# Performance work log

Measured on AMD Instinct MI355X. Metric: run time of the kernel, lower is better.

The kernel has to match this reference:

```python
import jax, jax.numpy as jnp
import numpy as np

L_OUT, B, N, C, M, D, T = 4, 4, 1000, 80, 64, 256, 28
CLS_W, L1_W, GIOU_W, MASK_W = 2.0, 5.0, 2.0, 5.0
ALPHA, GAMMA, EPS = 0.25, 2.0, 1e-8
CANDIDATE_K, CENTER_RADIUS, BIG = 10, 2.5, 100000.0


def _areas(b):
    return (b[..., 2] - b[..., 0]) * (b[..., 3] - b[..., 1])


def pairwise_giou(b1, b2):
    # b1 [n,4], b2 [m,4] -> [n,m] generalized IoU (torchvision convention)
    area1, area2 = _areas(b1), _areas(b2)
    lt = jnp.maximum(b1[:, None, :2], b2[None, :, :2])
    rb = jnp.minimum(b1[:, None, 2:], b2[None, :, 2:])
    wh = jnp.clip(rb - lt, 0.0)
    inter = wh[..., 0] * wh[..., 1]
    union = area1[:, None] + area2[None, :] - inter
    iou = inter / union
    lti = jnp.minimum(b1[:, None, :2], b2[None, :, :2])
    rbi = jnp.maximum(b1[:, None, 2:], b2[None, :, 2:])
    whi = jnp.clip(rbi - lti, 0.0)
    areai = whi[..., 0] * whi[..., 1]
    return iou - (areai - union) / areai


def diag_giou(b1, b2):
    # elementwise giou for matched pairs, b1/b2 [n,4] -> [n]
    area1, area2 = _areas(b1), _areas(b2)
    lt = jnp.maximum(b1[:, :2], b2[:, :2])
    rb = jnp.minimum(b1[:, 2:], b2[:, 2:])
    wh = jnp.clip(rb - lt, 0.0)
    inter = wh[:, 0] * wh[:, 1]
    union = area1 + area2 - inter
    iou = inter / union
    lti = jnp.minimum(b1[:, :2], b2[:, :2])
    rbi = jnp.maximum(b1[:, 2:], b2[:, 2:])
    whi = jnp.clip(rbi - lti, 0.0)
    areai = whi[:, 0] * whi[:, 1]
    return iou - (areai - union) / areai


def pairwise_iou(b1, b2, eps=1e-8):
    # mmdet bbox_overlaps, mode='iou'
    area1, area2 = _areas(b1), _areas(b2)
    lt = jnp.maximum(b1[:, None, :2], b2[None, :, :2])
    rb = jnp.minimum(b1[:, None, 2:], b2[None, :, 2:])
    wh = jnp.clip(rb - lt, 0.0)
    inter = wh[..., 0] * wh[..., 1]
    union = jnp.maximum(area1[:, None] + area2[None, :] - inter, eps)
    return inter / union


def simota_match(logits, boxes, gt_cls, gt_boxes, img_size):
    # SimOTA assignment for one image; fixed shapes via masking instead of boolean indexing
    n, c = logits.shape
    m = gt_boxes.shape[0]
    cx = (boxes[:, 0] + boxes[:, 2]) * 0.5
    cy = (boxes[:, 1] + boxes[:, 3]) * 0.5
    w = boxes[:, 2] - boxes[:, 0]
    h = boxes[:, 3] - boxes[:, 1]
    in_gt = ((cx[:, None] > gt_boxes[None, :, 0]) & (cy[:, None] > gt_boxes[None, :, 1])
             & (cx[:, None] < gt_boxes[None, :, 2]) & (cy[:, None] < gt_boxes[None, :, 3]))
    gcx = (gt_boxes[:, 0] + gt_boxes[:, 2]) * 0.5
    gcy = (gt_boxes[:, 1] + gt_boxes[:, 3]) * 0.5
    rx = CENTER_RADIUS * w[:, None]
    ry = CENTER_RADIUS * h[:, None]
    in_ct = ((cx[:, None] > gcx[None, :] - rx) & (cx[:, None] < gcx[None, :] + rx)
             & (cy[:, None] > gcy[None, :] - ry) & (cy[:, None] < gcy[None, :] + ry))
    valid = in_gt.any(1) | in_ct.any(1)
    in_both = in_gt & in_ct
    has_valid = valid.any()
    valid = valid | (~has_valid)          # fallback: all valid when none
    in_both = in_both | (~has_valid)
    # FocalLossCost (mmdet), weight = cls weight
    p = jax.nn.sigmoid(logits)
    neg = -jnp.log(1.0 - p + EPS) * (1.0 - ALPHA) * p ** GAMMA
    pos = -jnp.log(p + EPS) * ALPHA * (1.0 - p) ** GAMMA
    cls_cost = CLS_W * (pos - neg)[:, gt_cls]          # [n,m]
    nb = boxes / img_size
    ngb = gt_boxes / img_size
    l1_cost = L1_W * jnp.abs(nb[:, None, :] - ngb[None, :, :]).sum(-1)
    giou_cost = GIOU_W * (1.0 - pairwise_giou(nb, ngb))
    cost = cls_cost + l1_cost + giou_cost + (~in_both) * BIG
    cost = jnp.where(valid[:, None], cost, 1e15)       # invalid priors never selected
    ious = pairwise_iou(boxes, gt_boxes) * valid[:, None]
    # dynamic_k_matching
    topk_ious, _ = jax.lax.top_k(ious.T, CANDIDATE_K)  # [m,10]
    dyn_k = jnp.maximum(topk_ious.sum(-1).astype(jnp.int32), 1)
    rank = jnp.argsort(jnp.argsort(cost, axis=0), axis=0)
    matching = rank < dyn_k[None, :]                   # [n,m]
    multi = matching.sum(1) > 1
    best = jnp.argmin(cost, axis=1)
    best_oh = best[:, None] == jnp.arange(m)[None, :]
    matching = jnp.where(multi[:, None], best_oh, matching)
    fg = matching.any(1)
    gt_ind = jnp.argmax(matching, axis=1)
    return fg, gt_ind


def per_image_loss(logits, boxes, pfeat, gt_cls, gt_boxes, gt_masks, img_size, w_mask):
    sg = jax.lax.stop_gradient
    fg, gt_ind = simota_match(sg(logits), sg(boxes), gt_cls, sg(gt_boxes), sg(img_size))
    c = logits.shape[1]
    gcls = gt_cls[gt_ind]
    label = jnp.where(fg[:, None], jax.nn.one_hot(gcls, c, dtype=logits.dtype), 0.0)
    # sigmoid focal loss (sum over all n*c logits)
    p = jax.nn.sigmoid(logits)
    ce = -(label * jax.nn.log_sigmoid(logits) + (1.0 - label) * jax.nn.log_sigmoid(-logits))
    p_t = p * label + (1.0 - p) * (1.0 - label)
    alpha_t = ALPHA * label + (1.0 - ALPHA) * (1.0 - label)
    cls_loss = (alpha_t * ce * (1.0 - p_t) ** GAMMA).sum()
    fgf = fg.astype(logits.dtype)
    nb = boxes / img_size
    gb = gt_boxes[gt_ind] / img_size
    l1_loss = (jnp.abs(nb - gb).sum(-1) * fgf).sum()
    giou_loss = ((1.0 - diag_giou(nb, gb)) * fgf).sum()
    # mask head: per-class mask logits from proposal feats; gather only assigned class
    d = pfeat.shape[1]
    tt = T * T
    w_sel = w_mask.reshape(d, c, tt)[:, gcls, :]        # [d,n,tt]
    m_sel = jax.nn.sigmoid(jnp.einsum('nd,dnt->nt', pfeat, w_sel))
    gm = gt_masks.reshape(gt_masks.shape[0], -1)[gt_ind]  # [n,tt]
    inter = (m_sel * gm).sum(-1)
    union = m_sel.sum(-1) + gm.sum(-1) + 1e-8
    mask_loss = ((1.0 - 2.0 * inter / union) * fgf).sum()
    return cls_loss, l1_loss, giou_loss, mask_loss, fgf.sum()


def _forward(pred_logits, pred_boxes, proposal_feat, gt_boxes, gt_masks, image_size, w_mask, gt_classes):
    per = jax.vmap(per_image_loss, in_axes=(0, 0, 0, 0, 0, 0, 0, None))
    total = jnp.zeros(4, dtype=pred_logits.dtype)
    n_out = pred_logits.shape[0]
    for l in range(n_out):   # small fixed loop over output heads
        cl, l1, gl, ml, k = per(pred_logits[l], pred_boxes[l], proposal_feat[l],
                                gt_classes, gt_boxes, gt_masks, image_size, w_mask)
        num_ins = k.sum()
        total = total + jnp.stack([cl.sum(), l1.sum(), gl.sum(), ml.sum()]) / num_ins
    weights = jnp.array([CLS_W, L1_W, GIOU_W, MASK_W], dtype=total.dtype)
    return weights * total / n_out   # [cls, l1, giou, mask] losses


def setup_inputs():
    key = jax.random.key(0)
    ks = jax.random.split(key, 8)

    def rand_boxes(k, shape):
        k1, k2 = jax.random.split(k)
        ctr = jax.random.uniform(k1, shape + (2,), minval=100.0, maxval=700.0)
        wh = jax.random.uniform(k2, shape + (2,), minval=20.0, maxval=300.0)
        return jnp.concatenate([ctr - wh * 0.5, ctr + wh * 0.5], axis=-1)

    pred_logits = jax.random.normal(ks[0], (L_OUT, B, N, C), dtype=jnp.float32)
    pred_boxes = rand_boxes(ks[1], (L_OUT, B, N))
    proposal_feat = 0.1 * jax.random.normal(ks[2], (L_OUT, B, N, D), dtype=jnp.float32)
    gt_boxes = rand_boxes(ks[3], (B, M))
    gt_masks = (jax.random.uniform(ks[4], (B, M, T, T)) > 0.5).astype(jnp.float32)
    image_size = 800.0 * jnp.ones((B,), dtype=jnp.float32)
    w_mask = 0.02 * jax.random.normal(ks[5], (D, C * T * T), dtype=jnp.float32)
    gt_classes = jax.random.randint(ks[6], (B, M), 0, C)
    return {"pred_logits": pred_logits, "pred_boxes": pred_boxes, "proposal_feat": proposal_feat,
            "gt_boxes": gt_boxes, "gt_masks": gt_masks, "image_size": image_size,
            "w_mask": w_mask, "gt_classes": gt_classes}


def reference(pred_logits, pred_boxes, proposal_feat, gt_boxes, gt_masks, image_size, w_mask, gt_classes):
    return _forward(pred_logits, pred_boxes, proposal_feat, gt_boxes, gt_masks, image_size, w_mask, gt_classes)
```

## Files before the change

### kernel.cpp

```cpp
#include <hip/hip_runtime.h>
#include <math.h>
#include <float.h>

#define LOUT 4
#define BATCH 4
#define NP 1000
#define NC 80
#define NM 64
#define ND 256
#define TT 784
#define NIMG (LOUT*BATCH)
#define CWTT (NC*TT)
#define MAXF (NIMG*NP)
#define CH 32
#define TPT 112
#define MAXCH 408

__device__ __forceinline__ float block_reduce_sum(float v, float* red) {
    int tid = threadIdx.x;
    red[tid] = v; __syncthreads();
    for (int s = blockDim.x >> 1; s > 0; s >>= 1) {
        if (tid < s) red[tid] += red[tid + s];
        __syncthreads();
    }
    float r = red[0]; __syncthreads();
    return r;
}

__global__ void k_valid(const float* __restrict__ boxes, const float* __restrict__ gtb,
                        int* __restrict__ valid, unsigned long long* __restrict__ inboth,
                        int* __restrict__ hasvalid) {
    int img = blockIdx.y;
    int b = img % BATCH;
    int i = blockIdx.x * blockDim.x + threadIdx.x;
    __shared__ float g[NM * 4];
    for (int k = threadIdx.x; k < NM * 4; k += blockDim.x) g[k] = gtb[b * NM * 4 + k];
    __syncthreads();
    if (i >= NP) return;
    float4 bx = *(const float4*)&boxes[((size_t)img * NP + i) * 4];
    float x0 = bx.x, y0 = bx.y, x1 = bx.z, y1 = bx.w;
    float cx = (x0 + x1) * 0.5f, cy = (y0 + y1) * 0.5f;
    float w = x1 - x0, h = y1 - y0;
    float rx = 2.5f * w, ry = 2.5f * h;
    bool any_gt = false, any_ct = false;
    unsigned long long ib = 0ull;
    for (int j = 0; j < NM; ++j) {
        float gx0 = g[j*4], gy0 = g[j*4+1], gx1 = g[j*4+2], gy1 = g[j*4+3];
        bool igt = (cx > gx0) && (cy > gy0) && (cx < gx1) && (cy < gy1);
        float gcx = (gx0 + gx1) * 0.5f, gcy = (gy0 + gy1) * 0.5f;
        bool ict = (cx > gcx - rx) && (cx < gcx + rx) && (cy > gcy - ry) && (cy < gcy + ry);
        any_gt |= igt; any_ct |= ict;
        if (igt && ict) ib |= (1ull << j);
    }
    bool v = any_gt || any_ct;
    valid[img * NP + i] = v ? 1 : 0;
    inboth[img * NP + i] = ib;
    if (v) atomicOr(&hasvalid[img], 1);
}

__global__ void __launch_bounds__(256) k_costtopk(
        const float* __restrict__ logits, const float* __restrict__ boxes,
        const float* __restrict__ gtb, const int* __restrict__ gcls_all,
        const float* __restrict__ imsz,
        const int* __restrict__ valid, const unsigned long long* __restrict__ inboth,
        const int* __restrict__ hasvalid,
        float* __restrict__ cost, float* __restrict__ kthc, int* __restrict__ kthi) {
    int j = blockIdx.x, img = blockIdx.y, b = img % BATCH;
    float s = imsz[b], inv_s = 1.f / s;
    const float* gj = gtb + (b * NM + j) * 4;
    float gx0 = gj[0], gy0 = gj[1], gx1 = gj[2], gy1 = gj[3];
    int gc = gcls_all[b * NM + j];
    int hv = hasvalid[img];
    float garea = (gx1 - gx0) * (gy1 - gy0);
    float ngx0 = gx0 * inv_s, ngy0 = gy0 * inv_s, ngx1 = gx1 * inv_s, ngy1 = gy1 * inv_s;
    float ngarea = (ngx1 - ngx0) * (ngy1 - ngy0);
    size_t colbase = ((size_t)img * NM + j) * NP;
    int tid = threadIdx.x;
    float icv[4], ccv[4];
    #pragma unroll
    for (int e = 0; e < 4; ++e) {
        int i = tid + 256 * e;
        if (i < NP) {
            float4 bx = *(const float4*)&boxes[((size_t)img * NP + i) * 4];
            float x0 = bx.x, y0 = bx.y, x1 = bx.z, y1 = bx.w;
            float area = (x1 - x0) * (y1 - y0);
            float ltx = fmaxf(x0, gx0), lty = fmaxf(y0, gy0);
            float rbx = fminf(x1, gx1), rby = fminf(y1, gy1);
            float iw = fmaxf(rbx - ltx, 0.f), ih = fmaxf(rby - lty, 0.f);
            float inter = iw * ih;
            float uni = fmaxf(area + garea - inter, 1e-8f);
            float iou = inter / uni;
            float nx0 = x0 * inv_s, ny0 = y0 * inv_s, nx1 = x1 * inv_s, ny1 = y1 * inv_s;
            float narea = (nx1 - nx0) * (ny1 - ny0);
            float nltx = fmaxf(nx0, ngx0), nlty = fmaxf(ny0, ngy0);
            float nrbx = fminf(nx1, ngx1), nrby = fminf(ny1, ngy1);
            float niw = fmaxf(nrbx - nltx, 0.f), nih = fmaxf(nrby - nlty, 0.f);
            float ninter = niw * nih;
            float nuni = narea + ngarea - ninter;
            float niou = ninter / nuni;
            float ex0 = fminf(nx0, ngx0), ey0 = fminf(ny0, ngy0);
            float ex1 = fmaxf(nx1, ngx1), ey1 = fmaxf(ny1, ngy1);
            float earea = fmaxf(ex1 - ex0, 0.f) * fmaxf(ey1 - ey0, 0.f);
            float giou = niou - (earea - nuni) / earea;
            float giou_cost = 2.f * (1.f - giou);
            float l1 = 5.f * (fabsf(nx0 - ngx0) + fabsf(ny0 - ngy0) + fabsf(nx1 - ngx1) + fabsf(ny1 - ngy1));
            float x = logits[((size_t)img * NP + i) * NC + gc];
            float p = 1.f / (1.f + expf(-x));
            float neg = -logf(1.f - p + 1e-8f) * 0.75f * p * p;
            float pos = -logf(p + 1e-8f) * 0.25f * (1.f - p) * (1.f - p);
            float cls = 2.f * (pos - neg);
            bool vld = (valid[img * NP + i] != 0) || (hv == 0);
            bool inb = (((inboth[img * NP + i] >> j) & 1ull) != 0ull) || (hv == 0);
            float cst = cls + l1 + giou_cost + (inb ? 0.f : 100000.f);
            if (!vld) cst = 1e15f;
            cost[colbase + i] = cst;
            ccv[e] = cst;
            icv[e] = vld ? iou : 0.f;
        } else {
            ccv[e] = FLT_MAX;
            icv[e] = -FLT_MAX;
        }
    }
    __shared__ float wv[4]; __shared__ int wi[4];
    int wave = tid >> 6, lane = tid & 63;
    unsigned cons = 0;
    float ssum = 0.f;
    for (int it = 0; it < 10; ++it) {
        float bv = -FLT_MAX; int bi = NP;
        #pragma unroll
        for (int e = 0; e < 4; ++e) {
            int i = tid + 256 * e;
            float v = icv[e];
            if (!(cons & (1u << e)) && ((v > bv) || (v == bv && i < bi))) { bv = v; bi = i; }
        }
        #pragma unroll
        for (int sft = 1; sft < 64; sft <<= 1) {
            float ov = __shfl_xor(bv, sft, 64);
            int oi = __shfl_xor(bi, sft, 64);
            if ((ov > bv) || (ov == bv && oi < bi)) { bv = ov; bi = oi; }
        }
        if (lane == 0) { wv[wave] = bv; wi[wave] = bi; }
        __syncthreads();
        float gv = wv[0]; int gi = wi[0];
        #pragma unroll
        for (int w = 1; w < 4; ++w) {
            float ov = wv[w]; int oi = wi[w];
            if ((ov > gv) || (ov == gv && oi < gi)) { gv = ov; gi = oi; }
        }
        __syncthreads();
        ssum += gv;
        if ((gi & 255) == tid) cons |= (1u << (gi >> 8));
    }
    int dk = (int)ssum; if (dk < 1) dk = 1;
    cons = 0;
    float gvf = 0.f; int gif = 0;
    for (int it = 0; it < dk; ++it) {
        float bv = FLT_MAX; int bi = NP;
        #pragma unroll
        for (int e = 0; e < 4; ++e) {
            int i = tid + 256 * e;
            float v = ccv[e];
            if (!(cons & (1u << e)) && ((v < bv) || (v == bv && i < bi))) { bv = v; bi = i; }
        }
        #pragma unroll
        for (int sft = 1; sft < 64; sft <<= 1) {
            float ov = __shfl_xor(bv, sft, 64);
            int oi = __shfl_xor(bi, sft, 64);
            if ((ov < bv) || (ov == bv && oi < bi)) { bv = ov; bi = oi; }
        }
        if (lane == 0) { wv[wave] = bv; wi[wave] = bi; }
        __syncthreads();
        float gv = wv[0]; int gi = wi[0];
        #pragma unroll
        for (int w = 1; w < 4; ++w) {
            float ov = wv[w]; int oi = wi[w];
            if ((ov < gv) || (ov == gv && oi < gi)) { gv = ov; gi = oi; }
        }
        __syncthreads();
        if ((gi & 255) == tid) cons |= (1u << (gi >> 8));
        gvf = gv; gif = gi;
    }
    if (tid == 0) { kthc[blockIdx.y * NM + j] = gvf; kthi[blockIdx.y * NM + j] = gif; }
}

__global__ void k_match(const float* __restrict__ cost,
                        const float* __restrict__ kthc, const int* __restrict__ kthi,
                        const float* __restrict__ boxes, const float* __restrict__ gtb,
                        const float* __restrict__ imsz, const int* __restrict__ gcls_all,
                        int* __restrict__ fg, int* __restrict__ gt_ind,
                        int* __restrict__ cnt, float* __restrict__ accum) {
    int img = blockIdx.y, b = img % BATCH;
    int i = blockIdx.x * blockDim.x + threadIdx.x;
    __shared__ float skc[NM]; __shared__ int ski[NM];
    __shared__ float red[256];
    if (threadIdx.x < NM) {
        skc[threadIdx.x] = kthc[img * NM + threadIdx.x];
        ski[threadIdx.x] = kthi[img * NM + threadIdx.x];
    }
    __syncthreads();
    float l1 = 0.f, gl = 0.f, f = 0.f;
    if (i < NP) {
        int cntm = 0, first = -1;
        float bc = FLT_MAX; int bj = 0;
        for (int j = 0; j < NM; ++j) {
            float c = cost[((size_t)img * NM + j) * NP + i];
            bool m = (c < skc[j]) || (c == skc[j] && i <= ski[j]);
            if (m) { cntm++; if (first < 0) first = j; }
            if (c < bc) { bc = c; bj = j; }
        }
        int gi = 0, isfg = 0;
        if (cntm > 1) { gi = bj; isfg = 1; }
        else if (cntm == 1) { gi = first; isfg = 1; }
        fg[img * NP + i] = isfg;
        gt_ind[img * NP + i] = gi;
        if (isfg) {
            atomicAdd(&cnt[gcls_all[b * NM + gi]], 1);
            float inv = 1.f / imsz[b];
            float4 bx = *(const float4*)&boxes[((size_t)img * NP + i) * 4];
            const float* gj = gtb + (b * NM + gi) * 4;
            float nx0 = bx.x*inv, ny0 = bx.y*inv, nx1 = bx.z*inv, ny1 = bx.w*inv;
            float gx0 = gj[0]*inv, gy0 = gj[1]*inv, gx1 = gj[2]*inv, gy1 = gj[3]*inv;
            l1 = fabsf(nx0-gx0) + fabsf(ny0-gy0) + fabsf(nx1-gx1) + fabsf(ny1-gy1);
            float a1 = (nx1-nx0)*(ny1-ny0), a2 = (gx1-gx0)*(gy1-gy0);
            float ltx = fmaxf(nx0,gx0), lty = fmaxf(ny0,gy0);
            float rbx = fminf(nx1,gx1), rby = fminf(ny1,gy1);
            float iw = fmaxf(rbx-ltx,0.f), ih = fmaxf(rby-lty,0.f);
            float inter = iw*ih, uni = a1+a2-inter, iou = inter/uni;
            float ex0 = fminf(nx0,gx0), ey0 = fminf(ny0,gy0);
            float ex1 = fmaxf(nx1,gx1), ey1 = fmaxf(ny1,gy1);
            float ea = fmaxf(ex1-ex0,0.f)*fmaxf(ey1-ey0,0.f);
            float giou = iou - (ea-uni)/ea;
            gl = 1.f - giou;
            f = 1.f;
        }
    }
    float sl1 = block_reduce_sum(l1, red);
    float sgl = block_reduce_sum(gl, red);
    float sf  = block_reduce_sum(f, red);
    if (threadIdx.x == 0) {
        atomicAdd(&accum[img*5+1], sl1);
        atomicAdd(&accum[img*5+2], sgl);
        atomicAdd(&accum[img*5+4], sf);
    }
}

__global__ void k_focal(const float* __restrict__ logits, const int* __restrict__ fg,
                        const int* __restrict__ gt_ind, const int* __restrict__ gcls_all,
                        float* __restrict__ accum) {
    int img = blockIdx.y, b = img % BATCH;
    int idx = blockIdx.x * blockDim.x + threadIdx.x;
    __shared__ float red[256];
    float v = 0.f;
    if (idx < NP * NC) {
        int i = idx / NC, c = idx % NC;
        float x = logits[(size_t)img * NP * NC + idx];
        int lab = 0;
        if (fg[img * NP + i]) {
            int gc = gcls_all[b * NM + gt_ind[img * NP + i]];
            lab = (c == gc) ? 1 : 0;
        }
        float p = 1.f / (1.f + expf(-x));
        float ax = fabsf(x);
        float sp = log1pf(expf(-ax));
        float ls_pos = fminf(x, 0.f) - sp;
        float ls_neg = fminf(-x, 0.f) - sp;
        if (lab) v = 0.25f * (-ls_pos) * (1.f - p) * (1.f - p);
        else     v = 0.75f * (-ls_neg) * p * p;
    }
    float sv = block_reduce_sum(v, red);
    if (threadIdx.x == 0) atomicAdd(&accum[img*5+0], sv);
}

__global__ void k_gmsum(const float* __restrict__ gtm, float* __restrict__ gmsum) {
    int bj = blockIdx.x;
    __shared__ float red[128];
    float s = 0.f;
    for (int t = threadIdx.x; t < TT; t += 128) s += gtm[(size_t)bj * TT + t];
    int tid = threadIdx.x;
    red[tid] = s; __syncthreads();
    for (int st = 64; st > 0; st >>= 1) {
        if (tid < st) red[tid] += red[tid + st];
        __syncthreads();
    }
    if (tid == 0) gmsum[bj] = red[0];
}

__global__ void __launch_bounds__(1024) k_scanscatter(
        const int* __restrict__ cnt, const int* __restrict__ fg,
        const int* __restrict__ gti, const int* __restrict__ gcls,
        int* __restrict__ offs_g, int* __restrict__ total,
        int* __restrict__ chtab, int* __restrict__ nch, int* __restrict__ list) {
    __shared__ int offs[NC]; __shared__ int choff[NC]; __shared__ int sfill[NC];
    int tid = threadIdx.x;
    if (tid == 0) {
        int s = 0, m = 0;
        for (int c = 0; c < NC; ++c) {
            offs[c] = s; s += cnt[c];
            choff[c] = m; m += (cnt[c] + CH - 1) / CH;
        }
        *total = s; *nch = m;
    }
    if (tid < NC) sfill[tid] = 0;
    __syncthreads();
    if (tid < NC) {
        offs_g[tid] = offs[tid];
        int n = cnt[tid], co = choff[tid];
        for (int k = 0; k * CH < n; ++k) chtab[co + k] = (tid << 16) | k;
    }
    for (int idx = tid; idx < NIMG * NP; idx += 1024) {
        if (fg[idx]) {
            int img = idx / NP, i = idx % NP, b = img % BATCH;
            int gt = gti[idx];
            int c = gcls[b * NM + gt];
            int pos = offs[c] + atomicAdd(&sfill[c], 1);
            list[pos] = (img << 16) | (gt << 10) | i;
        }
    }
}

__global__ void __launch_bounds__(128) k_mgemm(
        const float* __restrict__ pfeat, const float* __restrict__ wmask,
        const float* __restrict__ gtm, const int* __restrict__ list,
        const int* __restrict__ cnt, const int* __restrict__ offs,
        const int* __restrict__ chtab, const int* __restrict__ nch,
        float* __restrict__ inter, float* __restrict__ msum) {
    int ch = blockIdx.x;
    if (ch >= *nch) return;
    int e = chtab[ch];
    int c = e >> 16, k = e & 0xffff;
    int base = offs[c] + k * CH;
    int P = min(CH, cnt[c] - k * CH);
    int tid = threadIdx.x;
    bool act = (tid < TPT);
    int t = blockIdx.y * TPT + (act ? tid : 0);
    __shared__ float pf[CH][ND];
    __shared__ int sl[CH];
    if (tid < CH) sl[tid] = (tid < P) ? list[base + tid] : 0;
    __syncthreads();
    for (int idx = tid; idx < CH * (ND / 4); idx += 128) {
        int p = idx >> 6, d4 = idx & 63;
        float4 v = {0.f, 0.f, 0.f, 0.f};
        if (p < P) {
            int pk = sl[p];
            int img = pk >> 16, i = pk & 1023;
            v = *(const float4*)&pfeat[((size_t)img * NP + i) * ND + d4 * 4];
        }
        *(float4*)&pf[p][d4 * 4] = v;
    }
    __syncthreads();
    float acc[CH];
    #pragma unroll
    for (int p = 0; p < CH; ++p) acc[p] = 0.f;
    if (act) {
        const float* wr = wmask + (size_t)c * TT + t;
        float4 wq[4];
        #pragma unroll
        for (int q = 0; q < 4; ++q) {
            const float* wp = wr + (size_t)q * 4 * CWTT;
            wq[q].x = wp[0]; wq[q].y = wp[CWTT];
            wq[q].z = wp[2 * (size_t)CWTT]; wq[q].w = wp[3 * (size_t)CWTT];
        }
        #pragma unroll 4
        for (int d4 = 0; d4 < 60; ++d4) {
            float4 w = wq[d4 & 3];
            const float* wp = wr + (size_t)(d4 + 4) * 4 * CWTT;
            wq[d4 & 3].x = wp[0]; wq[d4 & 3].y = wp[CWTT];
            wq[d4 & 3].z = wp[2 * (size_t)CWTT]; wq[d4 & 3].w = wp[3 * (size_t)CWTT];
            int d = d4 * 4;
            #pragma unroll
            for (int p = 0; p < CH; ++p) {
                float4 q4 = *(const float4*)&pf[p][d];
                acc[p] += q4.x * w.x + q4.y * w.y + q4.z * w.z + q4.w * w.w;
            }
        }
        #pragma unroll
        for (int d4 = 60; d4 < 64; ++d4) {
            float4 w = wq[d4 & 3];
            int d = d4 * 4;
            #pragma unroll
            for (int p = 0; p < CH; ++p) {
                float4 q4 = *(const float4*)&pf[p][d];
                acc[p] += q4.x * w.x + q4.y * w.y + q4.z * w.z + q4.w * w.w;
            }
        }
    }
    #pragma unroll 4
    for (int p = 0; p < CH; ++p) {
        if (p >= P) break;
        int pk = sl[p];
        int img = pk >> 16, j = (pk >> 10) & 63, b = img % BATCH;
        float li = 0.f, lm = 0.f;
        if (act) {
            float m = 1.f / (1.f + expf(-acc[p]));
            float g = gtm[((size_t)(b * NM + j)) * TT + t];
            li = m * g; lm = m;
        }
        #pragma unroll
        for (int s = 32; s > 0; s >>= 1) {
            li += __shfl_down(li, s, 64);
            lm += __shfl_down(lm, s, 64);
        }
        if ((tid & 63) == 0) {
            atomicAdd(&inter[base + p], li);
            atomicAdd(&msum[base + p], lm);
        }
    }
}

__global__ void __launch_bounds__(256) k_dicefinal(
        const int* __restrict__ list, const int* __restrict__ total,
        const float* __restrict__ inter, const float* __restrict__ msum,
        const float* __restrict__ gmsum, const float* __restrict__ accum,
        float* __restrict__ out) {
    __shared__ float md[NIMG];
    int tid = threadIdx.x;
    if (tid < NIMG) md[tid] = 0.f;
    __syncthreads();
    int n = *total;
    for (int e = tid; e < n; e += 256) {
        int pk = list[e];
        int img = pk >> 16, j = (pk >> 10) & 63, b = img % BATCH;
        float d = 1.f - 2.f * inter[e] / (msum[e] + gmsum[b * NM + j] + 1e-8f);
        atomicAdd(&md[img], d);
    }
    __syncthreads();
    if (tid == 0) {
        float tot[4] = {0.f, 0.f, 0.f, 0.f};
        for (int l = 0; l < LOUT; ++l) {
            float s0 = 0.f, s1 = 0.f, s2 = 0.f, s3 = 0.f, s4 = 0.f;
            for (int b = 0; b < BATCH; ++b) {
                int img = l * BATCH + b;
                s0 += accum[img*5+0]; s1 += accum[img*5+1]; s2 += accum[img*5+2];
                s3 += md[img];        s4 += accum[img*5+4];
            }
            tot[0] += s0 / s4; tot[1] += s1 / s4; tot[2] += s2 / s4; tot[3] += s3 / s4;
        }
        const float w[4] = {2.f, 5.f, 2.f, 5.f};
        for (int k = 0; k < 4; ++k) out[k] = w[k] * tot[k] / (float)LOUT;
    }
}

extern "C" void kernel_launch(void* const* d_in, const int* in_sizes, int n_in,
                              void* d_out, int out_size, void* d_ws, size_t ws_size,
                              hipStream_t stream) {
    const float* logits = (const float*)d_in[0];
    const float* boxes  = (const float*)d_in[1];
    const float* pfeat  = (const float*)d_in[2];
    const float* gtb    = (const float*)d_in[3];
    const float* gtm    = (const float*)d_in[4];
    const float* imsz   = (const float*)d_in[5];
    const float* wmask  = (const float*)d_in[6];
    const int*   gcls   = (const int*)d_in[7];

    char* ws = (char*)d_ws;
    size_t off = 0;
    auto alloc = [&](size_t bytes) -> void* {
        void* p = ws + off;
        off = (off + bytes + 255) & ~(size_t)255;
        return p;
    };
    char* zbase = ws;
    float* accum = (float*)alloc(NIMG * 5 * sizeof(float));
    int* cnt    = (int*)alloc(NC * sizeof(int));
    int* hasvalid = (int*)alloc(NIMG * sizeof(int));
    float* interA = (float*)alloc((size_t)MAXF * sizeof(float));
    float* msumA  = (float*)alloc((size_t)MAXF * sizeof(float));
    size_t zbytes = off;
    float* cost = (float*)alloc((size_t)NIMG * NM * NP * sizeof(float));
    int* valid  = (int*)alloc((size_t)NIMG * NP * sizeof(int));
    unsigned long long* inboth = (unsigned long long*)alloc((size_t)NIMG * NP * sizeof(unsigned long long));
    float* kthc = (float*)alloc(NIMG * NM * sizeof(float));
    int* kthi   = (int*)alloc(NIMG * NM * sizeof(int));
    int* fg     = (int*)alloc((size_t)NIMG * NP * sizeof(int));
    int* gti    = (int*)alloc((size_t)NIMG * NP * sizeof(int));
    float* gmsum = (float*)alloc(BATCH * NM * sizeof(float));
    int* offs   = (int*)alloc(NC * sizeof(int));
    int* total  = (int*)alloc(sizeof(int));
    int* nch    = (int*)alloc(sizeof(int));
    int* chtab  = (int*)alloc((size_t)MAXCH * sizeof(int));
    int* list   = (int*)alloc((size_t)MAXF * sizeof(int));

    hipMemsetAsync(zbase, 0, zbytes, stream);

    k_gmsum<<<BATCH * NM, 128, 0, stream>>>(gtm, gmsum);
    k_valid<<<dim3((NP + 255) / 256, NIMG), 256, 0, stream>>>(boxes, gtb, valid, inboth, hasvalid);
    k_costtopk<<<dim3(NM, NIMG), 256, 0, stream>>>(logits, boxes, gtb, gcls, imsz, valid, inboth, hasvalid, cost, kthc, kthi);
    k_match<<<dim3((NP + 255) / 256, NIMG), 256, 0, stream>>>(cost, kthc, kthi, boxes, gtb, imsz, gcls, fg, gti, cnt, accum);
    k_focal<<<dim3((NP * NC + 255) / 256, NIMG), 256, 0, stream>>>(logits, fg, gti, gcls, accum);
    k_scanscatter<<<1, 1024, 0, stream>>>(cnt, fg, gti, gcls, offs, total, chtab, nch, list);
    k_mgemm<<<dim3(MAXCH, (TT + TPT - 1) / TPT), 128, 0, stream>>>(pfeat, wmask, gtm, list, cnt, offs, chtab, nch, interA, msumA);
    k_dicefinal<<<1, 256, 0, stream>>>(list, total, interA, msumA, gmsum, accum, (float*)d_out);
}
```

Measured before the change: 237.4 us.

## Split mask GEMM over feature dim, add parallel dice reduce and transposed logits

```diff
diff --git a/kernel.cpp b/kernel.cpp
--- a/kernel.cpp
+++ b/kernel.cpp
@@ -12,9 +12,10 @@
 #define NIMG (LOUT*BATCH)
 #define CWTT (NC*TT)
 #define MAXF (NIMG*NP)
-#define CH 32
+#define CAPF 10240
+#define CH 16
 #define TPT 112
-#define MAXCH 408
+#define MAXCH 768
 
 __device__ __forceinline__ float block_reduce_sum(float v, float* red) {
     int tid = threadIdx.x;
@@ -58,8 +59,22 @@
     if (v) atomicOr(&hasvalid[img], 1);
 }
 
+__global__ void k_logT(const float* __restrict__ logits, float* __restrict__ logT) {
+    __shared__ float tile[32][33];
+    int img = blockIdx.z;
+    int i0 = blockIdx.x * 32, c0 = blockIdx.y * 32;
+    int tx = threadIdx.x, ty = threadIdx.y;
+    int i = i0 + ty, c = c0 + tx;
+    float v = 0.f;
+    if (i < NP && c < NC) v = logits[((size_t)img * NP + i) * NC + c];
+    tile[ty][tx] = v;
+    __syncthreads();
+    int co = c0 + ty, io = i0 + tx;
+    if (co < NC && io < NP) logT[((size_t)img * NC + co) * NP + io] = tile[tx][ty];
+}
+
 __global__ void __launch_bounds__(256) k_costtopk(
-        const float* __restrict__ logits, const float* __restrict__ boxes,
+        const float* __restrict__ logT, const float* __restrict__ boxes,
         const float* __restrict__ gtb, const int* __restrict__ gcls_all,
         const float* __restrict__ imsz,
         const int* __restrict__ valid, const unsigned long long* __restrict__ inboth,
@@ -75,6 +90,7 @@
     float ngx0 = gx0 * inv_s, ngy0 = gy0 * inv_s, ngx1 = gx1 * inv_s, ngy1 = gy1 * inv_s;
     float ngarea = (ngx1 - ngx0) * (ngy1 - ngy0);
     size_t colbase = ((size_t)img * NM + j) * NP;
+    const float* lrow = logT + ((size_t)img * NC + gc) * NP;
     int tid = threadIdx.x;
     float icv[4], ccv[4];
     #pragma unroll
@@ -104,7 +120,7 @@
             float giou = niou - (earea - nuni) / earea;
             float giou_cost = 2.f * (1.f - giou);
             float l1 = 5.f * (fabsf(nx0 - ngx0) + fabsf(ny0 - ngy0) + fabsf(nx1 - ngx1) + fabsf(ny1 - ngy1));
-            float x = logits[((size_t)img * NP + i) * NC + gc];
+            float x = lrow[i];
             float p = 1.f / (1.f + expf(-x));
             float neg = -logf(1.f - p + 1e-8f) * 0.75f * p * p;
             float pos = -logf(p + 1e-8f) * 0.25f * (1.f - p) * (1.f - p);
@@ -318,7 +334,125 @@
     }
 }
 
-__global__ void __launch_bounds__(128) k_mgemm(
+template<int DQ>
+__global__ void __launch_bounds__(128) k_mgemmQ(
+        const float* __restrict__ pfeat, const float* __restrict__ wmask,
+        const int* __restrict__ list, const int* __restrict__ cnt,
+        const int* __restrict__ offs, const int* __restrict__ chtab,
+        const int* __restrict__ nch, float* __restrict__ part) {
+    constexpr int DL = ND / DQ;
+    constexpr int NSTEP = DL / 4;
+    int ch = blockIdx.x;
+    if (ch >= *nch) return;
+    int e = chtab[ch];
+    int c = e >> 16, k = e & 0xffff;
+    int base = offs[c] + k * CH;
+    int P = min(CH, cnt[c] - k * CH);
+    int tid = threadIdx.x;
+    int q = blockIdx.z;
+    int dbase = q * DL;
+    bool act = (tid < TPT);
+    int t = blockIdx.y * TPT + (act ? tid : 0);
+    __shared__ float pf[CH][DL];
+    __shared__ int sl[CH];
+    if (tid < CH) sl[tid] = (tid < P) ? list[base + tid] : 0;
+    __syncthreads();
+    for (int idx = tid; idx < CH * (DL / 4); idx += 128) {
+        int p = idx / (DL / 4), d4 = idx % (DL / 4);
+        float4 v = {0.f, 0.f, 0.f, 0.f};
+        if (p < P) {
+            int pk = sl[p];
+            int img = pk >> 16, i = pk & 1023;
+            v = *(const float4*)&pfeat[((size_t)img * NP + i) * ND + dbase + d4 * 4];
+        }
+        *(float4*)&pf[p][d4 * 4] = v;
+    }
+    __syncthreads();
+    float acc[CH];
+    #pragma unroll
+    for (int p = 0; p < CH; ++p) acc[p] = 0.f;
+    if (act) {
+        const float* wr = wmask + (size_t)dbase * CWTT + (size_t)c * TT + t;
+        float4 wq[4];
+        #pragma unroll
+        for (int qq = 0; qq < 4; ++qq) {
+            const float* wp = wr + (size_t)qq * 4 * CWTT;
+            wq[qq].x = wp[0]; wq[qq].y = wp[CWTT];
+            wq[qq].z = wp[2 * (size_t)CWTT]; wq[qq].w = wp[3 * (size_t)CWTT];
+        }
+        #pragma unroll 4
+        for (int d4 = 0; d4 < NSTEP - 4; ++d4) {
+            float4 w = wq[d4 & 3];
+            const float* wp = wr + (size_t)(d4 + 4) * 4 * CWTT;
+            wq[d4 & 3].x = wp[0]; wq[d4 & 3].y = wp[CWTT];
+            wq[d4 & 3].z = wp[2 * (size_t)CWTT]; wq[d4 & 3].w = wp[3 * (size_t)CWTT];
+            int d = d4 * 4;
+            #pragma unroll
+            for (int p = 0; p < CH; ++p) {
+                float4 q4 = *(const float4*)&pf[p][d];
+                acc[p] += q4.x * w.x + q4.y * w.y + q4.z * w.z + q4.w * w.w;
+            }
+        }
+        #pragma unroll
+        for (int d4 = NSTEP - 4; d4 < NSTEP; ++d4) {
+            float4 w = wq[d4 & 3];
+            int d = d4 * 4;
+            #pragma unroll
+            for (int p = 0; p < CH; ++p) {
+                float4 q4 = *(const float4*)&pf[p][d];
+                acc[p] += q4.x * w.x + q4.y * w.y + q4.z * w.z + q4.w * w.w;
+            }
+        }
+        float* pq = part + (size_t)q * CAPF * TT + (size_t)base * TT + t;
+        #pragma unroll
+        for (int p = 0; p < CH; ++p) {
+            if (p < P) pq[(size_t)p * TT] = acc[p];
+        }
+    }
+}
+
+__global__ void __launch_bounds__(256) k_dice2(
+        const float* __restrict__ part, const int* __restrict__ list,
+        const int* __restrict__ total, const float* __restrict__ gtm,
+        const float* __restrict__ gmsum, float* __restrict__ accum, int dq) {
+    int e = blockIdx.x;
+    if (e >= *total) return;
+    int pk = list[e];
+    int img = pk >> 16, j = (pk >> 10) & 63, b = img % BATCH;
+    __shared__ float red[256];
+    int tid = threadIdx.x;
+    float li = 0.f, lm = 0.f;
+    const float* gr = gtm + ((size_t)(b * NM + j)) * TT;
+    for (int t = tid; t < TT; t += 256) {
+        float x = 0.f;
+        for (int q = 0; q < dq; ++q) x += part[(size_t)q * CAPF * TT + (size_t)e * TT + t];
+        float m = 1.f / (1.f + expf(-x));
+        li += m * gr[t];
+        lm += m;
+    }
+    float I = block_reduce_sum(li, red);
+    float Ms = block_reduce_sum(lm, red);
+    if (tid == 0) {
+        float d = 1.f - 2.f * I / (Ms + gmsum[b * NM + j] + 1e-8f);
+        atomicAdd(&accum[img * 5 + 3], d);
+    }
+}
+
+__global__ void k_final(const float* __restrict__ accum, float* __restrict__ out) {
+    if (threadIdx.x == 0 && blockIdx.x == 0) {
+        float tot[4] = {0.f, 0.f, 0.f, 0.f};
+        for (int l = 0; l < LOUT; ++l) {
+            float s[5] = {0.f, 0.f, 0.f, 0.f, 0.f};
+            for (int b = 0; b < BATCH; ++b)
+                for (int k = 0; k < 5; ++k) s[k] += accum[(l * BATCH + b) * 5 + k];
+            for (int k = 0; k < 4; ++k) tot[k] += s[k] / s[4];
+        }
+        const float w[4] = {2.f, 5.f, 2.f, 5.f};
+        for (int k = 0; k < 4; ++k) out[k] = w[k] * tot[k] / (float)LOUT;
+    }
+}
+
+__global__ void __launch_bounds__(128) k_mgemm_legacy(
         const float* __restrict__ pfeat, const float* __restrict__ wmask,
         const float* __restrict__ gtm, const int* __restrict__ list,
         const int* __restrict__ cnt, const int* __restrict__ offs,
@@ -467,6 +601,7 @@
     float* msumA  = (float*)alloc((size_t)MAXF * sizeof(float));
     size_t zbytes = off;
     float* cost = (float*)alloc((size_t)NIMG * NM * NP * sizeof(float));
+    float* logT = (float*)alloc((size_t)NIMG * NC * NP * sizeof(float));
     int* valid  = (int*)alloc((size_t)NIMG * NP * sizeof(int));
     unsigned long long* inboth = (unsigned long long*)alloc((size_t)NIMG * NP * sizeof(unsigned long long));
     float* kthc = (float*)alloc(NIMG * NM * sizeof(float));
@@ -479,15 +614,34 @@
     int* nch    = (int*)alloc(sizeof(int));
     int* chtab  = (int*)alloc((size_t)MAXCH * sizeof(int));
     int* list   = (int*)alloc((size_t)MAXF * sizeof(int));
+    size_t slab1 = (size_t)CAPF * TT * sizeof(float);
+    size_t avail = (ws_size > off) ? (ws_size - off) : 0;
+    int DQ = 0;
+    if (avail >= 4 * slab1) DQ = 4;
+    else if (avail >= 2 * slab1) DQ = 2;
+    else if (avail >= slab1) DQ = 1;
+    float* part = (float*)(ws + off);
 
     hipMemsetAsync(zbase, 0, zbytes, stream);
 
     k_gmsum<<<BATCH * NM, 128, 0, stream>>>(gtm, gmsum);
     k_valid<<<dim3((NP + 255) / 256, NIMG), 256, 0, stream>>>(boxes, gtb, valid, inboth, hasvalid);
-    k_costtopk<<<dim3(NM, NIMG), 256, 0, stream>>>(logits, boxes, gtb, gcls, imsz, valid, inboth, hasvalid, cost, kthc, kthi);
+    k_logT<<<dim3((NP + 31) / 32, (NC + 31) / 32, NIMG), dim3(32, 32), 0, stream>>>(logits, logT);
+    k_costtopk<<<dim3(NM, NIMG), 256, 0, stream>>>(logT, boxes, gtb, gcls, imsz, valid, inboth, hasvalid, cost, kthc, kthi);
     k_match<<<dim3((NP + 255) / 256, NIMG), 256, 0, stream>>>(cost, kthc, kthi, boxes, gtb, imsz, gcls, fg, gti, cnt, accum);
     k_focal<<<dim3((NP * NC + 255) / 256, NIMG), 256, 0, stream>>>(logits, fg, gti, gcls, accum);
     k_scanscatter<<<1, 1024, 0, stream>>>(cnt, fg, gti, gcls, offs, total, chtab, nch, list);
-    k_mgemm<<<dim3(MAXCH, (TT + TPT - 1) / TPT), 128, 0, stream>>>(pfeat, wmask, gtm, list, cnt, offs, chtab, nch, interA, msumA);
-    k_dicefinal<<<1, 256, 0, stream>>>(list, total, interA, msumA, gmsum, accum, (float*)d_out);
-}
+    if (DQ > 0) {
+        if (DQ == 4)
+            k_mgemmQ<4><<<dim3(MAXCH, 7, 4), 128, 0, stream>>>(pfeat, wmask, list, cnt, offs, chtab, nch, part);
+        else if (DQ == 2)
+            k_mgemmQ<2><<<dim3(MAXCH, 7, 2), 128, 0, stream>>>(pfeat, wmask, list, cnt, offs, chtab, nch, part);
+        else
+            k_mgemmQ<1><<<dim3(MAXCH, 7, 1), 128, 0, stream>>>(pfeat, wmask, list, cnt, offs, chtab, nch, part);
+        k_dice2<<<CAPF, 256, 0, stream>>>(part, list, total, gtm, gmsum, accum, DQ);
+        k_final<<<1, 64, 0, stream>>>(accum, (float*)d_out);
+    } else {
+        k_mgemm_legacy<<<dim3(MAXCH, 7), 128, 0, stream>>>(pfeat, wmask, gtm, list, cnt, offs, chtab, nch, interA, msumA);
+        k_dicefinal<<<1, 256, 0, stream>>>(list, total, interA, msumA, gmsum, accum, (float*)d_out);
+    }
+}
```

New measurement: 293.0 us. 1.23x slower.
